# Optimization experiments

Measured on AMD Instinct MI355X. Metric: run time of the kernel, lower is better.

Reference implementation:

```python
import jax, jax.numpy as jnp
import numpy as np

SIGMA_MAX = 25.0

def marginal_prob_std(t):
    # VE-SDE std: sqrt((sigma_max^(2t) - 1) / (2 ln sigma_max))
    log_s = jnp.log(SIGMA_MAX)
    return jnp.sqrt((jnp.exp(2.0 * t * log_s) - 1.0) / (2.0 * log_s))

def setup_inputs() -> dict:
    key = jax.random.key(0)
    k1, k2, k3 = jax.random.split(key, 3)
    B, N, d = 16384, 16384, 1
    x = jax.random.normal(k1, (B, d), dtype=jnp.float32)
    t = jax.random.uniform(k2, (B,), dtype=jnp.float32, minval=1e-3, maxval=1.0)
    train_data = jax.random.normal(k3, (N, d), dtype=jnp.float32)
    return {"x": x, "t": t, "train_data": train_data}

def reference(x, t, train_data):
    # x: [B,1], t: [B], train_data: [N,1]
    sigma = marginal_prob_std(t)                       # [B]
    sigma2 = sigma * sigma                             # [B]
    # pairwise squared distance (d=1): [N, B]
    diff = train_data - x[:, 0][None, :]               # [N,1]-[1,B] -> broadcast fails; do explicit
    diff = train_data[:, 0][:, None] - x[:, 0][None, :]  # [N, B]
    pdf = jnp.exp(-0.5 * (diff * diff) / sigma2[None, :])  # [N, B]
    num = jnp.sum(pdf * train_data, axis=0)            # [N,B]*[N,1] -> [B]
    den = jnp.sum(pdf, axis=0)                         # [B]
    den_safe = jnp.where(den == 0.0, 1.0, den)
    evals = jnp.where(den == 0.0, 0.0, num / den_safe) # nan -> 0 as in torch code
    evals = evals[:, None]                             # [B,1]
    return (evals - x) / sigma2[:, None]
```

## Files before the change

### kernel.cpp

```cpp
#include <hip/hip_runtime.h>
#include <math.h>


typedef float v2f __attribute__((ext_vector_type(2)));

#define BLK   256
#define CH    512

#if __has_builtin(__builtin_amdgcn_exp2f)
#define EXP2(x) __builtin_amdgcn_exp2f(x)
#else
#define EXP2(x) exp2f(x)
#endif

__device__ __forceinline__ float sigma2_of(float tj) {
  const float TWO_LOG_S = 6.4377516497364011f;
  return (__expf(TWO_LOG_S * tj) - 1.0f) / TWO_LOG_S;
}

template <bool ATOMIC>
__launch_bounds__(BLK)
__global__ void gmm_partial(const float* __restrict__ x,
                            const float* __restrict__ t,
                            const float* __restrict__ td,
                            float* __restrict__ ws,
                            int N, int B) {
  __shared__ float lds[CH];
  const int tid  = threadIdx.x;
  const int j    = blockIdx.x * BLK + tid;
  const int s    = blockIdx.y;
  const int S    = gridDim.y;
  const int base = s * CH;

  for (int i = tid; i < CH; i += BLK) {
    int gi = base + i;
    lds[i] = (gi < N) ? td[gi] : 1e30f;
  }

  float r = 0.0f, y = 0.0f;
  if (j < B) {
    const float HALF_LOG2E = 0.72134752044448170f;
    float s2 = sigma2_of(t[j]);
    r = __fsqrt_rn(HALF_LOG2E / s2);
    y = x[j] * r;
  }
  __syncthreads();

  const v2f rv  = {r, r};
  const v2f nyv = {-y, -y};
  v2f num0 = {0.f, 0.f}, num1 = {0.f, 0.f}, num2 = {0.f, 0.f}, num3 = {0.f, 0.f};
  v2f den0 = {0.f, 0.f}, den1 = {0.f, 0.f}, den2 = {0.f, 0.f}, den3 = {0.f, 0.f};

  const float4* l4 = (const float4*)lds;
  const int iters = CH >> 3;
  #pragma unroll 2
  for (int i = 0; i < iters; ++i) {
    float4 v0 = l4[2 * i];
    float4 v1 = l4[2 * i + 1];
    v2f va = {v0.x, v0.y}, vb = {v0.z, v0.w};
    v2f vc = {v1.x, v1.y}, vd = {v1.z, v1.w};
    v2f da = __builtin_elementwise_fma(va, rv, nyv);
    v2f db = __builtin_elementwise_fma(vb, rv, nyv);
    v2f dc = __builtin_elementwise_fma(vc, rv, nyv);
    v2f dd = __builtin_elementwise_fma(vd, rv, nyv);
    v2f qa = da * da;
    v2f qb = db * db;
    v2f qc = dc * dc;
    v2f qd = dd * dd;
    v2f pa, pb, pc, pd;
    pa.x = EXP2(-qa.x); pa.y = EXP2(-qa.y);
    pb.x = EXP2(-qb.x); pb.y = EXP2(-qb.y);
    pc.x = EXP2(-qc.x); pc.y = EXP2(-qc.y);
    pd.x = EXP2(-qd.x); pd.y = EXP2(-qd.y);
    den0 += pa;
    den1 += pb;
    den2 += pc;
    den3 += pd;
    num0 = __builtin_elementwise_fma(pa, va, num0);
    num1 = __builtin_elementwise_fma(pb, vb, num1);
    num2 = __builtin_elementwise_fma(pc, vc, num2);
    num3 = __builtin_elementwise_fma(pd, vd, num3);
  }
  v2f numv = (num0 + num1) + (num2 + num3);
  v2f denv = (den0 + den1) + (den2 + den3);
  float num = numv.x + numv.y;
  float den = denv.x + denv.y;

  if (j < B) {
    if (ATOMIC) {
      atomicAdd(&ws[j], num);
      atomicAdd(&ws[B + j], den);
    } else {
      ws[(size_t)s * B + j]       = num;
      ws[(size_t)(S + s) * B + j] = den;
    }
  }
}

#define FJ 32
#define FG 8
__launch_bounds__(FJ * FG)
__global__ void gmm_final(const float* __restrict__ x,
                          const float* __restrict__ t,
                          const float* __restrict__ ws,
                          float* __restrict__ out, int B, int S) {
  __shared__ float nbuf[FG * FJ];
  __shared__ float dbuf[FG * FJ];
  const int tid = threadIdx.x;
  const int jl  = tid & (FJ - 1);
  const int g   = tid >> 5;
  const int j   = blockIdx.x * FJ + jl;

  float np = 0.f, dp = 0.f;
  if (j < B) {
    for (int s = g; s < S; s += FG) {
      np += ws[(size_t)s * B + j];
      dp += ws[(size_t)(S + s) * B + j];
    }
  }
  nbuf[tid] = np;
  dbuf[tid] = dp;
  __syncthreads();

  if (g == 0 && j < B) {
    float num = 0.f, den = 0.f;
    #pragma unroll
    for (int gg = 0; gg < FG; ++gg) {
      num += nbuf[gg * FJ + jl];
      den += dbuf[gg * FJ + jl];
    }
    float sigma2 = sigma2_of(t[j]);
    float evals = (den == 0.0f) ? 0.0f : (num / den);
    out[j] = (evals - x[j]) / sigma2;
  }
}

__global__ void gmm_final_serial(const float* __restrict__ x,
                                 const float* __restrict__ t,
                                 const float* __restrict__ ws,
                                 float* __restrict__ out, int B, int S) {
  int j = blockIdx.x * blockDim.x + threadIdx.x;
  if (j >= B) return;
  float num = 0.f, den = 0.f;
  for (int s = 0; s < S; ++s) {
    num += ws[(size_t)s * B + j];
    den += ws[(size_t)(S + s) * B + j];
  }
  float sigma2 = sigma2_of(t[j]);
  float evals = (den == 0.0f) ? 0.0f : (num / den);
  out[j] = (evals - x[j]) / sigma2;
}

__global__ void zero_kernel(float* __restrict__ p, int n) {
  int i = blockIdx.x * blockDim.x + threadIdx.x;
  if (i < n) p[i] = 0.0f;
}

extern "C" void kernel_launch(void* const* d_in, const int* in_sizes, int n_in,
                              void* d_out, int out_size, void* d_ws, size_t ws_size,
                              hipStream_t stream) {
  const float* x  = (const float*)d_in[0];
  const float* t  = (const float*)d_in[1];
  const float* td = (const float*)d_in[2];
  float* out = (float*)d_out;
  float* ws  = (float*)d_ws;

  const int B = in_sizes[0];
  const int N = in_sizes[2];

  const int S = (N + CH - 1) / CH;
  size_t need = (size_t)2 * S * B * sizeof(float);

  if (ws_size >= need) {
    dim3 grid((B + BLK - 1) / BLK, S);
    gmm_partial<false><<<grid, BLK, 0, stream>>>(x, t, td, ws, N, B);
    gmm_final<<<(B + FJ - 1) / FJ, FJ * FG, 0, stream>>>(x, t, ws, out, B, S);
  } else {
    int nzero = 2 * B;
    zero_kernel<<<(nzero + 255) / 256, 256, 0, stream>>>(ws, nzero);
    dim3 grid((B + BLK - 1) / BLK, S);
    gmm_partial<true><<<grid, BLK, 0, stream>>>(x, t, td, ws, N, B);
    gmm_final_serial<<<(B + 255) / 256, 256, 0, stream>>>(x, t, ws, out, B, 1);
  }
}
```

Measured before the change: 92.82 us.

## Fuse partial reduction and finalize into one kernel with in-block split over N

Replaces the two-kernel scheme with a single kernel. The old scheme wrote per-chunk partial sums to a workspace, then ran a separate final reduction kernel. In the new kernel each block owns 16 query points and splits the training data into 16 parts across its threads, reading training values straight from global memory instead of staging them in LDS. Partial sums are combined in shared memory and the output is written directly, which removes the workspace traffic and the second launch. In exchange there are fewer independent accumulators, and each wavefront issues redundant global loads that rely on cache hits.

```diff
diff --git a/kernel.cpp b/kernel.cpp
--- a/kernel.cpp
+++ b/kernel.cpp
@@ -5,7 +5,8 @@
 typedef float v2f __attribute__((ext_vector_type(2)));
 
 #define BLK   256
-#define CH    512
+#define JB    16
+#define PARTS 16
 
 #if __has_builtin(__builtin_amdgcn_exp2f)
 #define EXP2(x) __builtin_amdgcn_exp2f(x)
@@ -18,24 +19,23 @@
   return (__expf(TWO_LOG_S * tj) - 1.0f) / TWO_LOG_S;
 }
 
-template <bool ATOMIC>
-__launch_bounds__(BLK)
-__global__ void gmm_partial(const float* __restrict__ x,
-                            const float* __restrict__ t,
-                            const float* __restrict__ td,
-                            float* __restrict__ ws,
-                            int N, int B) {
-  __shared__ float lds[CH];
+__launch_bounds__(BLK, 4)
+__global__ void gmm_fused(const float* __restrict__ x,
+                          const float* __restrict__ t,
+                          const float* __restrict__ td,
+                          float* __restrict__ out,
+                          int N, int B) {
+  __shared__ float nbuf[PARTS * JB];
+  __shared__ float dbuf[PARTS * JB];
+
   const int tid  = threadIdx.x;
-  const int j    = blockIdx.x * BLK + tid;
-  const int s    = blockIdx.y;
-  const int S    = gridDim.y;
-  const int base = s * CH;
+  const int jl   = tid & (JB - 1);
+  const int part = tid >> 4;
+  const int j    = blockIdx.x * JB + jl;
 
-  for (int i = tid; i < CH; i += BLK) {
-    int gi = base + i;
-    lds[i] = (gi < N) ? td[gi] : 1e30f;
-  }
+  const int W  = (N + PARTS - 1) / PARTS;
+  const int lo = part * W;
+  const int hi = (lo + W < N) ? (lo + W) : N;
 
   float r = 0.0f, y = 0.0f;
   if (j < B) {
@@ -44,116 +44,64 @@
     r = __fsqrt_rn(HALF_LOG2E / s2);
     y = x[j] * r;
   }
-  __syncthreads();
 
   const v2f rv  = {r, r};
   const v2f nyv = {-y, -y};
-  v2f num0 = {0.f, 0.f}, num1 = {0.f, 0.f}, num2 = {0.f, 0.f}, num3 = {0.f, 0.f};
-  v2f den0 = {0.f, 0.f}, den1 = {0.f, 0.f}, den2 = {0.f, 0.f}, den3 = {0.f, 0.f};
 
-  const float4* l4 = (const float4*)lds;
-  const int iters = CH >> 3;
-  #pragma unroll 2
-  for (int i = 0; i < iters; ++i) {
-    float4 v0 = l4[2 * i];
-    float4 v1 = l4[2 * i + 1];
-    v2f va = {v0.x, v0.y}, vb = {v0.z, v0.w};
-    v2f vc = {v1.x, v1.y}, vd = {v1.z, v1.w};
-    v2f da = __builtin_elementwise_fma(va, rv, nyv);
-    v2f db = __builtin_elementwise_fma(vb, rv, nyv);
-    v2f dc = __builtin_elementwise_fma(vc, rv, nyv);
-    v2f dd = __builtin_elementwise_fma(vd, rv, nyv);
-    v2f qa = da * da;
-    v2f qb = db * db;
-    v2f qc = dc * dc;
-    v2f qd = dd * dd;
-    v2f pa, pb, pc, pd;
-    pa.x = EXP2(-qa.x); pa.y = EXP2(-qa.y);
-    pb.x = EXP2(-qb.x); pb.y = EXP2(-qb.y);
-    pc.x = EXP2(-qc.x); pc.y = EXP2(-qc.y);
-    pd.x = EXP2(-qd.x); pd.y = EXP2(-qd.y);
-    den0 += pa;
-    den1 += pb;
-    den2 += pc;
-    den3 += pd;
-    num0 = __builtin_elementwise_fma(pa, va, num0);
-    num1 = __builtin_elementwise_fma(pb, vb, num1);
-    num2 = __builtin_elementwise_fma(pc, vc, num2);
-    num3 = __builtin_elementwise_fma(pd, vd, num3);
+  v2f n0 = {0.f, 0.f}, n1 = {0.f, 0.f};
+  v2f d0 = {0.f, 0.f}, d1 = {0.f, 0.f};
+
+#define GROUP(v, nacc, dacc)                                            \
+  {                                                                     \
+    v2f dd = __builtin_elementwise_fma(v, rv, nyv);                     \
+    v2f qq = dd * dd;                                                   \
+    v2f pp;                                                             \
+    pp.x = EXP2(-qq.x); pp.y = EXP2(-qq.y);                             \
+    dacc += pp;                                                         \
+    nacc = __builtin_elementwise_fma(pp, v, nacc);                      \
   }
-  v2f numv = (num0 + num1) + (num2 + num3);
-  v2f denv = (den0 + den1) + (den2 + den3);
-  float num = numv.x + numv.y;
-  float den = denv.x + denv.y;
 
-  if (j < B) {
-    if (ATOMIC) {
-      atomicAdd(&ws[j], num);
-      atomicAdd(&ws[B + j], den);
-    } else {
-      ws[(size_t)s * B + j]       = num;
-      ws[(size_t)(S + s) * B + j] = den;
+  int i = lo;
+  if (((W & 3) == 0)) {
+    const int hi8 = lo + ((hi - lo) & ~7);
+    #pragma unroll 2
+    for (; i < hi8; i += 8) {
+      float4 v0 = *(const float4*)(td + i);
+      float4 v1 = *(const float4*)(td + i + 4);
+      v2f va = {v0.x, v0.y}, vb = {v0.z, v0.w};
+      v2f vc = {v1.x, v1.y}, vd = {v1.z, v1.w};
+      GROUP(va, n0, d0)
+      GROUP(vb, n1, d1)
+      GROUP(vc, n0, d0)
+      GROUP(vd, n1, d1)
     }
   }
-}
+  for (; i < hi; i += 2) {
+    float e0 = td[i];
+    float e1 = (i + 1 < hi) ? td[i + 1] : 1e30f;
+    v2f v = {e0, e1};
+    GROUP(v, n0, d0)
+  }
+#undef GROUP
 
-#define FJ 32
-#define FG 8
-__launch_bounds__(FJ * FG)
-__global__ void gmm_final(const float* __restrict__ x,
-                          const float* __restrict__ t,
-                          const float* __restrict__ ws,
-                          float* __restrict__ out, int B, int S) {
-  __shared__ float nbuf[FG * FJ];
-  __shared__ float dbuf[FG * FJ];
-  const int tid = threadIdx.x;
-  const int jl  = tid & (FJ - 1);
-  const int g   = tid >> 5;
-  const int j   = blockIdx.x * FJ + jl;
-
-  float np = 0.f, dp = 0.f;
-  if (j < B) {
-    for (int s = g; s < S; s += FG) {
-      np += ws[(size_t)s * B + j];
-      dp += ws[(size_t)(S + s) * B + j];
-    }
-  }
-  nbuf[tid] = np;
-  dbuf[tid] = dp;
+  v2f numv = n0 + n1;
+  v2f denv = d0 + d1;
+  nbuf[part * JB + jl] = numv.x + numv.y;
+  dbuf[part * JB + jl] = denv.x + denv.y;
   __syncthreads();
 
-  if (g == 0 && j < B) {
+  if (tid < JB && (blockIdx.x * JB + tid) < B) {
+    const int jj = blockIdx.x * JB + tid;
     float num = 0.f, den = 0.f;
     #pragma unroll
-    for (int gg = 0; gg < FG; ++gg) {
-      num += nbuf[gg * FJ + jl];
-      den += dbuf[gg * FJ + jl];
+    for (int p = 0; p < PARTS; ++p) {
+      num += nbuf[p * JB + tid];
+      den += dbuf[p * JB + tid];
     }
-    float sigma2 = sigma2_of(t[j]);
+    float sigma2 = sigma2_of(t[jj]);
     float evals = (den == 0.0f) ? 0.0f : (num / den);
-    out[j] = (evals - x[j]) / sigma2;
+    out[jj] = (evals - x[jj]) / sigma2;
   }
-}
-
-__global__ void gmm_final_serial(const float* __restrict__ x,
-                                 const float* __restrict__ t,
-                                 const float* __restrict__ ws,
-                                 float* __restrict__ out, int B, int S) {
-  int j = blockIdx.x * blockDim.x + threadIdx.x;
-  if (j >= B) return;
-  float num = 0.f, den = 0.f;
-  for (int s = 0; s < S; ++s) {
-    num += ws[(size_t)s * B + j];
-    den += ws[(size_t)(S + s) * B + j];
-  }
-  float sigma2 = sigma2_of(t[j]);
-  float evals = (den == 0.0f) ? 0.0f : (num / den);
-  out[j] = (evals - x[j]) / sigma2;
-}
-
-__global__ void zero_kernel(float* __restrict__ p, int n) {
-  int i = blockIdx.x * blockDim.x + threadIdx.x;
-  if (i < n) p[i] = 0.0f;
 }
 
 extern "C" void kernel_launch(void* const* d_in, const int* in_sizes, int n_in,
@@ -163,23 +111,11 @@
   const float* t  = (const float*)d_in[1];
   const float* td = (const float*)d_in[2];
   float* out = (float*)d_out;
-  float* ws  = (float*)d_ws;
+  (void)d_ws; (void)ws_size;
 
   const int B = in_sizes[0];
   const int N = in_sizes[2];
 
-  const int S = (N + CH - 1) / CH;
-  size_t need = (size_t)2 * S * B * sizeof(float);
-
-  if (ws_size >= need) {
-    dim3 grid((B + BLK - 1) / BLK, S);
-    gmm_partial<false><<<grid, BLK, 0, stream>>>(x, t, td, ws, N, B);
-    gmm_final<<<(B + FJ - 1) / FJ, FJ * FG, 0, stream>>>(x, t, ws, out, B, S);
-  } else {
-    int nzero = 2 * B;
-    zero_kernel<<<(nzero + 255) / 256, 256, 0, stream>>>(ws, nzero);
-    dim3 grid((B + BLK - 1) / BLK, S);
-    gmm_partial<true><<<grid, BLK, 0, stream>>>(x, t, td, ws, N, B);
-    gmm_final_serial<<<(B + 255) / 256, 256, 0, stream>>>(x, t, ws, out, B, 1);
-  }
+  const int GX = (B + JB - 1) / JB;
+  gmm_fused<<<GX, BLK, 0, stream>>>(x, t, td, out, N, B);
 }
```

Result: slower. 95.13 us (+2.5%).
